# Performance work log

Hardware: AMD Instinct MI355X
Metric: run time of the kernel (lower is better)

## Reference

```python
import jax, jax.numpy as jnp
import numpy as np


def setup_inputs() -> dict:
    key = jax.random.key(0)
    k1, k2, k3 = jax.random.split(key, 3)
    B, T, D = 8, 2048, 128      # *A = (B, T), address_size = D
    N, V = 4096, 512            # num_addresses, *B = (V,)
    return {
        "selector": jax.random.normal(k1, (B, T, D), dtype=jnp.float32),
        "param_bank": jax.random.normal(k2, (N, V), dtype=jnp.float32),
        "address_space": jax.random.normal(k3, (N, D), dtype=jnp.float32),
    }


def reference(selector, param_bank, address_space):
    # scores: [B, T, N] = selector @ address_space^T (unscaled)
    scores = jnp.einsum("btd,nd->btn", selector, address_space)
    weights = jax.nn.softmax(scores, axis=-1)
    # weighted sum over the bank: [B, T, V]
    return jnp.einsum("btn,nv->btv", weights, param_bank)
```

## Files before the change

kernel.cpp:

```cpp
#include <hip/hip_runtime.h>

typedef __attribute__((ext_vector_type(8))) short bf16x8;
typedef __attribute__((ext_vector_type(8))) _Float16 f16x8;
typedef __attribute__((ext_vector_type(2))) __fp16 fp16v2;
typedef __attribute__((ext_vector_type(16))) float f32x16;

#define DDIM 128
#define NADDR 4096
#define VDIM 512
#define NT 32
#define ITERS (NADDR/NT)
#define LOG2E 1.44269504088896340736f

__device__ __forceinline__ unsigned pkhi(float hi, float lo){
  return __builtin_amdgcn_perm(__float_as_uint(hi), __float_as_uint(lo), 0x07060302u);
}

__global__ __launch_bounds__(256, 2)
void soft_addr_kernel(const float* __restrict__ sel,
                      const float* __restrict__ bank,
                      const float* __restrict__ addr,
                      float* __restrict__ out)
{
  __shared__ __align__(16) _Float16 sK[2][32][136];
  __shared__ __align__(16) short  sVt[2][128][40];
  __shared__ float sL[128];

  const int tid  = threadIdx.x;
  const int wave = tid >> 6;
  const int lane = tid & 63;
  const int h    = lane >> 5;
  const int c32  = lane & 31;

  const int bid  = blockIdx.x;
  const int vblk = bid & 3;
  const int mblk = bid >> 2;
  const int m0 = mblk * 128, v0 = vblk * 128;
  const int wm = wave * 32;

  f16x8 aQ[8];
  {
    const float* q = sel + (size_t)(m0 + wm + c32) * DDIM + 8*h;
    #pragma unroll
    for (int ks = 0; ks < 8; ++ks){
      float4 a = *(const float4*)(q + 16*ks);
      float4 b = *(const float4*)(q + 16*ks + 4);
      f16x8 f;
      f[0]=(_Float16)(a.x*LOG2E); f[1]=(_Float16)(a.y*LOG2E);
      f[2]=(_Float16)(a.z*LOG2E); f[3]=(_Float16)(a.w*LOG2E);
      f[4]=(_Float16)(b.x*LOG2E); f[5]=(_Float16)(b.y*LOG2E);
      f[6]=(_Float16)(b.z*LOG2E); f[7]=(_Float16)(b.w*LOG2E);
      aQ[ks] = f;
    }
  }

  f32x16 oAcc[4];
  #pragma unroll
  for (int jv=0;jv<4;++jv)
    #pragma unroll
    for (int r=0;r<16;++r) oAcc[jv][r] = 0.f;
  float lacc = 0.f;

  const int kr  = tid >> 4;
  const int kc  = (tid & 15) * 8;
  const int vv  = tid & 127;
  const int vnb = (tid >> 7) * 16;

  float4 kreg[2][2];
  float  vreg[16];

  {
    const float* ksrc = addr + (size_t)tid * 8;
    kreg[0][0] = *(const float4*)(ksrc);
    kreg[0][1] = *(const float4*)(ksrc + 4);
    kreg[1][0] = *(const float4*)(ksrc + 2048);
    kreg[1][1] = *(const float4*)(ksrc + 2052);
    const float* vsrc = bank + (size_t)vnb * VDIM + v0 + vv;
    #pragma unroll
    for (int k=0;k<16;++k) vreg[k] = vsrc[(size_t)k * VDIM];
  }

  for (int t = 0; t < ITERS; ++t){
    const int b = t & 1;

    #pragma unroll
    for (int c=0;c<2;++c){
      union { f16x8 v; fp16v2 hh[4]; } u;
      u.hh[0] = __builtin_amdgcn_cvt_pkrtz(kreg[c][0].x, kreg[c][0].y);
      u.hh[1] = __builtin_amdgcn_cvt_pkrtz(kreg[c][0].z, kreg[c][0].w);
      u.hh[2] = __builtin_amdgcn_cvt_pkrtz(kreg[c][1].x, kreg[c][1].y);
      u.hh[3] = __builtin_amdgcn_cvt_pkrtz(kreg[c][1].z, kreg[c][1].w);
      *(f16x8*)&sK[b][kr + 16*c][kc] = u.v;
    }
    {
      uint4 p0, p1;
      p0.x = pkhi(vreg[1],  vreg[0]);  p0.y = pkhi(vreg[3],  vreg[2]);
      p0.z = pkhi(vreg[5],  vreg[4]);  p0.w = pkhi(vreg[7],  vreg[6]);
      p1.x = pkhi(vreg[9],  vreg[8]);  p1.y = pkhi(vreg[11], vreg[10]);
      p1.z = pkhi(vreg[13], vreg[12]); p1.w = pkhi(vreg[15], vreg[14]);
      *(uint4*)&sVt[b][vv][vnb]     = p0;
      *(uint4*)&sVt[b][vv][vnb + 8] = p1;
    }

    __syncthreads();

    {
      const int n1 = ((t+1) & (ITERS-1)) * NT;
      const float* ksrc = addr + (size_t)n1 * DDIM + tid * 8;
      kreg[0][0] = *(const float4*)(ksrc);
      kreg[0][1] = *(const float4*)(ksrc + 4);
      kreg[1][0] = *(const float4*)(ksrc + 2048);
      kreg[1][1] = *(const float4*)(ksrc + 2052);
      const float* vsrc = bank + (size_t)(n1 + vnb) * VDIM + v0 + vv;
      #pragma unroll
      for (int k=0;k<16;++k) vreg[k] = vsrc[(size_t)k * VDIM];
    }

    f32x16 sAcc0, sAcc1;
    #pragma unroll
    for (int r=0;r<16;++r){ sAcc0[r] = 0.f; sAcc1[r] = 0.f; }
    #pragma unroll
    for (int ks=0; ks<4; ++ks){
      f16x8 aK0 = *(const f16x8*)&sK[b][c32][16*(2*ks)   + 8*h];
      f16x8 aK1 = *(const f16x8*)&sK[b][c32][16*(2*ks+1) + 8*h];
      sAcc0 = __builtin_amdgcn_mfma_f32_32x32x16_f16(aK0, aQ[2*ks],   sAcc0, 0,0,0);
      sAcc1 = __builtin_amdgcn_mfma_f32_32x32x16_f16(aK1, aQ[2*ks+1], sAcc1, 0,0,0);
    }

    unsigned dw[2][4];
    #pragma unroll
    for (int j=0;j<2;++j)
      #pragma unroll
      for (int i=0;i<4;++i){
        float pa = __builtin_amdgcn_exp2f(sAcc0[8*j + 2*i]     + sAcc1[8*j + 2*i]);
        float pb = __builtin_amdgcn_exp2f(sAcc0[8*j + 2*i + 1] + sAcc1[8*j + 2*i + 1]);
        lacc += __uint_as_float(__float_as_uint(pa) & 0xffff0000u);
        lacc += __uint_as_float(__float_as_uint(pb) & 0xffff0000u);
        dw[j][i] = pkhi(pb, pa);
      }

    #pragma unroll
    for (int j=0;j<2;++j){
      auto s02 = __builtin_amdgcn_permlane32_swap(dw[j][0], dw[j][2], false, false);
      auto s13 = __builtin_amdgcn_permlane32_swap(dw[j][1], dw[j][3], false, false);
      union { unsigned u[4]; bf16x8 v; } ap;
      ap.u[0] = s02[0]; ap.u[1] = s13[0]; ap.u[2] = s02[1]; ap.u[3] = s13[1];
      #pragma unroll
      for (int jv=0;jv<4;++jv){
        bf16x8 bV = *(const bf16x8*)&sVt[b][32*jv + c32][16*j + 8*h];
        oAcc[jv] = __builtin_amdgcn_mfma_f32_32x32x16_bf16(ap.v, bV, oAcc[jv], 0,0,0);
      }
    }
  }

  float tot = lacc + __shfl_xor(lacc, 32);
  if (lane < 32) sL[wm + c32] = tot;
  __syncthreads();

  #pragma unroll
  for (int r=0;r<16;++r){
    const int mrow = (r&3) + 8*(r>>2) + 4*h;
    const float inv = 1.0f / sL[wm + mrow];
    float* op = out + (size_t)(m0 + wm + mrow) * VDIM + v0 + c32;
    #pragma unroll
    for (int jv=0;jv<4;++jv)
      op[32*jv] = oAcc[jv][r] * inv;
  }
}

extern "C" void kernel_launch(void* const* d_in, const int* in_sizes, int n_in,
                              void* d_out, int out_size, void* d_ws, size_t ws_size,
                              hipStream_t stream) {
  const float* sel  = (const float*)d_in[0];
  const float* bank = (const float*)d_in[1];
  const float* addr = (const float*)d_in[2];
  float* out = (float*)d_out;
  dim3 grid(512), block(256);
  hipLaunchKernelGGL(soft_addr_kernel, grid, block, 0, stream, sel, bank, addr, out);
}
```

Baseline: 243.6 us.

## Compute softmax denominator via MFMA with ones vector and add wave priorities

```diff
diff --git a/kernel.cpp b/kernel.cpp
--- a/kernel.cpp
+++ b/kernel.cpp
@@ -24,7 +24,6 @@
 {
   __shared__ __align__(16) _Float16 sK[2][32][136];
   __shared__ __align__(16) short  sVt[2][128][40];
-  __shared__ float sL[128];
 
   const int tid  = threadIdx.x;
   const int wave = tid >> 6;
@@ -54,12 +53,23 @@
     }
   }
 
+  f32x16 zc;
+  #pragma unroll
+  for (int r=0;r<16;++r) zc[r] = 0.f;
+  asm volatile("" : "+v"(zc));
+  bf16x8 ones;
+  #pragma unroll
+  for (int i=0;i<8;++i) ones[i] = (short)0x3F80;
+  asm volatile("" : "+v"(ones));
+
   f32x16 oAcc[4];
   #pragma unroll
   for (int jv=0;jv<4;++jv)
     #pragma unroll
     for (int r=0;r<16;++r) oAcc[jv][r] = 0.f;
-  float lacc = 0.f;
+  f32x16 oDen;
+  #pragma unroll
+  for (int r=0;r<16;++r) oDen[r] = 0.f;
 
   const int kr  = tid >> 4;
   const int kc  = (tid & 15) * 8;
@@ -116,16 +126,22 @@
       for (int k=0;k<16;++k) vreg[k] = vsrc[(size_t)k * VDIM];
     }
 
+    __builtin_amdgcn_s_setprio(1);
     f32x16 sAcc0, sAcc1;
+    {
+      f16x8 aK0 = *(const f16x8*)&sK[b][c32][8*h];
+      f16x8 aK1 = *(const f16x8*)&sK[b][c32][16 + 8*h];
+      sAcc0 = __builtin_amdgcn_mfma_f32_32x32x16_f16(aK0, aQ[0], zc, 0,0,0);
+      sAcc1 = __builtin_amdgcn_mfma_f32_32x32x16_f16(aK1, aQ[1], zc, 0,0,0);
+    }
     #pragma unroll
-    for (int r=0;r<16;++r){ sAcc0[r] = 0.f; sAcc1[r] = 0.f; }
-    #pragma unroll
-    for (int ks=0; ks<4; ++ks){
+    for (int ks=1; ks<4; ++ks){
       f16x8 aK0 = *(const f16x8*)&sK[b][c32][16*(2*ks)   + 8*h];
       f16x8 aK1 = *(const f16x8*)&sK[b][c32][16*(2*ks+1) + 8*h];
       sAcc0 = __builtin_amdgcn_mfma_f32_32x32x16_f16(aK0, aQ[2*ks],   sAcc0, 0,0,0);
       sAcc1 = __builtin_amdgcn_mfma_f32_32x32x16_f16(aK1, aQ[2*ks+1], sAcc1, 0,0,0);
     }
+    __builtin_amdgcn_s_setprio(0);
 
     unsigned dw[2][4];
     #pragma unroll
@@ -134,8 +150,6 @@
       for (int i=0;i<4;++i){
         float pa = __builtin_amdgcn_exp2f(sAcc0[8*j + 2*i]     + sAcc1[8*j + 2*i]);
         float pb = __builtin_amdgcn_exp2f(sAcc0[8*j + 2*i + 1] + sAcc1[8*j + 2*i + 1]);
-        lacc += __uint_as_float(__float_as_uint(pa) & 0xffff0000u);
-        lacc += __uint_as_float(__float_as_uint(pb) & 0xffff0000u);
         dw[j][i] = pkhi(pb, pa);
       }
 
@@ -145,22 +159,21 @@
       auto s13 = __builtin_amdgcn_permlane32_swap(dw[j][1], dw[j][3], false, false);
       union { unsigned u[4]; bf16x8 v; } ap;
       ap.u[0] = s02[0]; ap.u[1] = s13[0]; ap.u[2] = s02[1]; ap.u[3] = s13[1];
+      __builtin_amdgcn_s_setprio(1);
+      oDen = __builtin_amdgcn_mfma_f32_32x32x16_bf16(ap.v, ones, oDen, 0,0,0);
       #pragma unroll
       for (int jv=0;jv<4;++jv){
         bf16x8 bV = *(const bf16x8*)&sVt[b][32*jv + c32][16*j + 8*h];
         oAcc[jv] = __builtin_amdgcn_mfma_f32_32x32x16_bf16(ap.v, bV, oAcc[jv], 0,0,0);
       }
+      __builtin_amdgcn_s_setprio(0);
     }
   }
-
-  float tot = lacc + __shfl_xor(lacc, 32);
-  if (lane < 32) sL[wm + c32] = tot;
-  __syncthreads();
 
   #pragma unroll
   for (int r=0;r<16;++r){
     const int mrow = (r&3) + 8*(r>>2) + 4*h;
-    const float inv = 1.0f / sL[wm + mrow];
+    const float inv = 1.0f / oDen[r];
     float* op = out + (size_t)(m0 + wm + mrow) * VDIM + v0 + c32;
     #pragma unroll
     for (int jv=0;jv<4;++jv)
```

New measurement: 251.7 us. 3.3% more time.
